# Performance work log

Hardware: AMD Instinct MI355X
Metric: run time of the kernel (lower is better)

## Reference

```python
import jax, jax.numpy as jnp
import numpy as np

E, D_MODEL, D_HIDDEN, N_TOKENS = 8, 1024, 4096, 16384


def setup_inputs() -> dict:
    key = jax.random.key(0)
    ks = jax.random.split(key, 6)
    inp = {
        "hidden_states": jax.random.normal(ks[0], (N_TOKENS, D_MODEL), jnp.float32),
        # tokens are pre-sorted by expert; equal-sized groups of N_TOKENS // E
        "fwd_expert_count": jnp.full((E,), N_TOKENS // E, dtype=jnp.int32),
        # weights stored [E, d_in, d_out] (math-equivalent transpose of torch's [E, out, in])
        "w_gelu": jax.random.normal(ks[1], (E, D_MODEL, D_HIDDEN), jnp.float32) * 0.02,
        "w_lin": jax.random.normal(ks[2], (E, D_MODEL, D_HIDDEN), jnp.float32) * 0.02,
        "b_lin": jax.random.normal(ks[3], (E, D_HIDDEN), jnp.float32) * 0.02,
        "w_o": jax.random.normal(ks[4], (E, D_HIDDEN, D_MODEL), jnp.float32) * 0.02,
        "b_o": jax.random.normal(ks[5], (E, D_MODEL), jnp.float32) * 0.02,
    }
    return inp


def reference(hidden_states, fwd_expert_count, w_gelu, w_lin, b_lin, w_o, b_o):
    # Grouped GEMM MoE expert FFN with gated GELU (T5DenseGatedActDense per expert).
    # setup_inputs uses equal group sizes, so the grouped GEMM is expressed as a
    # batched einsum over [E, capacity, d] blocks (tokens are sorted by expert).
    e, d_model, d_hidden = w_gelu.shape
    n = hidden_states.shape[0]
    cap = n // e  # per-expert token count (== fwd_expert_count[i])
    x = hidden_states.reshape(e, cap, d_model)
    # gate branch: no bias (FMoELinear bias=False), gelu_new (tanh approx)
    hidden_gelu = jax.nn.gelu(jnp.einsum('ecd,edh->ech', x, w_gelu), approximate=True)
    # linear branch: bias=True
    hidden_linear = jnp.einsum('ecd,edh->ech', x, w_lin) + b_lin[:, None, :]
    h = hidden_gelu * hidden_linear  # dropout is identity at inference
    out = jnp.einsum('ech,ehd->ecd', h, w_o) + b_o[:, None, :]
    return out.reshape(n, d_model)
```

## Files before the change

### kernel.cpp

```cpp
#include <hip/hip_runtime.h>

#define EXP 8
#define DM 1024
#define DH 4096
#define NT 16384

typedef __attribute__((ext_vector_type(8))) short bf16x8;
typedef __attribute__((ext_vector_type(4))) float f32x4;

static __device__ __forceinline__ unsigned short f2bf(float f) {
  unsigned int u = __float_as_uint(f);
  u = u + 0x7FFFu + ((u >> 16) & 1u);
  return (unsigned short)(u >> 16);
}

static __device__ __forceinline__ void gload_lds16(const void* g, void* l) {
  __builtin_amdgcn_global_load_lds((const __attribute__((address_space(1))) void*)g,
                                   (__attribute__((address_space(3))) void*)l, 16, 0, 0);
}

__global__ void cvt_bf16_k(const float* __restrict__ in, unsigned short* __restrict__ out,
                           long n4) {
  long i = (long)blockIdx.x * blockDim.x + threadIdx.x;
  const long stride = (long)gridDim.x * blockDim.x;
  for (; i < n4; i += stride) {
    const float4 v = ((const float4*)in)[i];
    ushort4 o;
    o.x = f2bf(v.x); o.y = f2bf(v.y); o.z = f2bf(v.z); o.w = f2bf(v.w);
    ((ushort4*)out)[i] = o;
  }
}

__global__ void transpose_cvt(const float* __restrict__ in, unsigned short* __restrict__ out,
                              int K, int N) {
  __shared__ float tile[32][33];
  const int n0 = blockIdx.x * 32, k0 = blockIdx.y * 32;
  const size_t boff = (size_t)blockIdx.z * K * N;
  const int tx = threadIdx.x, ty = threadIdx.y;
  const float* src = in + boff;
  unsigned short* dst = out + boff;
#pragma unroll
  for (int i = 0; i < 32; i += 8)
    tile[ty + i][tx] = src[(size_t)(k0 + ty + i) * N + n0 + tx];
  __syncthreads();
#pragma unroll
  for (int i = 0; i < 32; i += 8)
    dst[(size_t)(n0 + ty + i) * K + k0 + tx] = f2bf(tile[tx][ty + i]);
}


#define LDSA(row, chunk) lds[sb + (row) * 64 + ((((chunk) ^ ((row) & 7))) << 3)]
#define LDSB(row, chunk) lds[sb + 16384 + (row) * 64 + ((((chunk) ^ ((row) & 7))) << 3)]

#define RD_A(mh)                                                                   \
  _Pragma("unroll") for (int i = 0; i < 4; i++) _Pragma("unroll") for (int ks = 0; \
                                                                       ks < 2;    \
                                                                       ks++)      \
      fa[i][ks] = *(const bf16x8*)&LDSA(wr * 128 + (mh) * 64 + i * 16 + lrow, ks * 4 + khi);

#define RD_B(dst, jb)                                                              \
  _Pragma("unroll") for (int j = 0; j < 2; j++) _Pragma("unroll") for (int ks = 0; \
                                                                       ks < 2;    \
                                                                       ks++)      \
      dst[j][ks] = *(const bf16x8*)&LDSB(wc * 64 + ((jb) + j) * 16 + lrow, ks * 4 + khi);

#define MFMA16(mi, jb, fb)                                                        \
  __builtin_amdgcn_s_setprio(1);                                                  \
  _Pragma("unroll") for (int i = 0; i < 4; i++) _Pragma("unroll") for (int j = 0; \
                                                                       j < 2;    \
                                                                       j++)      \
      _Pragma("unroll") for (int ks = 0; ks < 2; ks++) acc[(mi) + i][(jb) + j] =  \
          __builtin_amdgcn_mfma_f32_16x16x32_bf16(fa[i][ks], fb[j][ks],           \
                                                  acc[(mi) + i][(jb) + j], 0, 0, 0); \
  __builtin_amdgcn_s_setprio(0);

#define BAR_FENCE()                      \
  __builtin_amdgcn_s_barrier();          \
  asm volatile("" ::: "memory");

__global__ __launch_bounds__(512, 1) void gemm1(
    const unsigned short* __restrict__ Xb,
    const unsigned short* __restrict__ WgT,
    const unsigned short* __restrict__ WlT,
    const float* __restrict__ b_lin,
    unsigned short* __restrict__ Hb) {
  __shared__ unsigned short lds[65536];

  const int t = threadIdx.x;
  const int nblk = blockIdx.x, mblk = blockIdx.y;
  const int e = mblk >> 3;
  const int m0 = mblk * 256, n0 = nblk * 128;

  const int lane = t & 63, wave = t >> 6;
  const int wr = wave >> 2, wc = wave & 3;
  const int lrow = lane & 15, khi = lane >> 4;

  const int presw = (((t & 7) ^ ((t >> 3) & 7)) << 3);
  const unsigned short* gAsrc = Xb + (size_t)(m0 + (t >> 3)) * DM + presw;
  const unsigned short* gGsrc = WgT + ((size_t)e * DH + n0 + (t >> 3)) * DM + presw;
  const unsigned short* gLsrc = WlT + ((size_t)e * DH + n0 + (t >> 3)) * DM + presw;

  const int KT = DM / 64;

  auto STAGE_A = [&](int kt, int half) {
    unsigned short* d = &lds[(kt & 1) * 32768 + half * 8192 + t * 8];
    const unsigned short* s = gAsrc + (size_t)(half * 128) * DM + kt * 64;
    gload_lds16(s, d);
    gload_lds16(s + (size_t)64 * DM, d + 4096);
  };
  auto STAGE_B = [&](int kt, int half) {
    unsigned short* d = &lds[(kt & 1) * 32768 + 16384 + half * 8192 + t * 8];
    const unsigned short* s = (half ? gLsrc : gGsrc) + kt * 64;
    gload_lds16(s, d);
    gload_lds16(s + (size_t)64 * DM, d + 4096);
  };

  f32x4 acc[8][4];
#pragma unroll
  for (int m = 0; m < 8; m++)
#pragma unroll
    for (int j = 0; j < 4; j++) acc[m][j] = 0.0f;

  STAGE_A(0, 0); STAGE_A(0, 1);
  STAGE_B(0, 0); STAGE_B(0, 1);
  STAGE_B(1, 0); STAGE_B(1, 1);
  asm volatile("s_waitcnt vmcnt(4)" ::: "memory");
  BAR_FENCE();

  for (int T = 0; T < KT; ++T) {
    const int sb = (T & 1) * 32768;
    bf16x8 fa[4][2], fb01[2][2], fb23[2][2];
    RD_A(0);
    RD_B(fb01, 0);
    if (T + 1 < KT) STAGE_A(T + 1, 0);
    __builtin_amdgcn_s_barrier();
    MFMA16(0, 0, fb01);
    BAR_FENCE();
    RD_B(fb23, 2);
    if (T + 1 < KT) STAGE_A(T + 1, 1);
    __builtin_amdgcn_s_barrier();
    MFMA16(0, 2, fb23);
    BAR_FENCE();
    RD_A(1);
    if (T + 2 < KT) STAGE_B(T + 2, 0);
    __builtin_amdgcn_s_barrier();
    MFMA16(4, 2, fb23);
    BAR_FENCE();
    if (T + 2 < KT) STAGE_B(T + 2, 1);
    __builtin_amdgcn_s_barrier();
    MFMA16(4, 0, fb01);
    if (T < KT - 2)       asm volatile("s_waitcnt vmcnt(4)" ::: "memory");
    else if (T == KT - 2) asm volatile("s_waitcnt vmcnt(0)" ::: "memory");
    BAR_FENCE();
  }

  __syncthreads();
  f32x4* ex = (f32x4*)lds;
  if (wc >= 2) {
    f32x4* dst = ex + (wr * 2 + (wc - 2)) * 2048;
#pragma unroll
    for (int m = 0; m < 8; m++)
#pragma unroll
      for (int j = 0; j < 4; j++) dst[(m * 4 + j) * 64 + lane] = acc[m][j];
  }
  __syncthreads();
  if (wc < 2) {
    const f32x4* src = ex + (wr * 2 + wc) * 2048;
#pragma unroll
    for (int m = 0; m < 8; m++) {
      const int rowbase = m0 + wr * 128 + (m >> 2) * 64 + (m & 3) * 16 + khi * 4;
#pragma unroll
      for (int j = 0; j < 4; j++) {
        const f32x4 l4 = src[(m * 4 + j) * 64 + lane];
        const int gcol = n0 + wc * 64 + j * 16 + lrow;
        const float bias = b_lin[(size_t)e * DH + gcol];
#pragma unroll
        for (int r = 0; r < 4; r++) {
          const float g = acc[m][j][r];
          const float li = l4[r] + bias;
          const float u = 0.7978845608028654f * (g + 0.044715f * g * g * g);
          const float th = 1.0f - 2.0f / (1.0f + __expf(2.0f * u));
          const float h = 0.5f * g * (1.0f + th) * li;
          Hb[(size_t)(rowbase + r) * DH + gcol] = f2bf(h);
        }
      }
    }
  }
}

__global__ __launch_bounds__(512, 1) void gemm2(
    const unsigned short* __restrict__ Hb,
    const unsigned short* __restrict__ WoT,
    const float* __restrict__ b_o,
    float* __restrict__ out) {
  __shared__ unsigned short lds[65536];

  const int t = threadIdx.x;
  const int nblk = blockIdx.x, mblk = blockIdx.y;
  const int e = mblk >> 3;
  const int m0 = mblk * 256, n0 = nblk * 256;

  const int lane = t & 63, wave = t >> 6;
  const int wr = wave >> 2, wc = wave & 3;
  const int lrow = lane & 15, khi = lane >> 4;

  const int presw = (((t & 7) ^ ((t >> 3) & 7)) << 3);
  const unsigned short* gAsrc = Hb + (size_t)(m0 + (t >> 3)) * DH + presw;
  const unsigned short* gBsrc = WoT + ((size_t)e * DM + n0 + (t >> 3)) * DH + presw;

  const int KT = DH / 64;

  auto STAGE_A = [&](int kt, int half) {
    unsigned short* d = &lds[(kt & 1) * 32768 + half * 8192 + t * 8];
    const unsigned short* s = gAsrc + (size_t)(half * 128) * DH + kt * 64;
    gload_lds16(s, d);
    gload_lds16(s + (size_t)64 * DH, d + 4096);
  };
  auto STAGE_B = [&](int kt, int half) {
    unsigned short* d = &lds[(kt & 1) * 32768 + 16384 + half * 8192 + t * 8];
    const unsigned short* s = gBsrc + (size_t)(half * 128) * DH + kt * 64;
    gload_lds16(s, d);
    gload_lds16(s + (size_t)64 * DH, d + 4096);
  };

  f32x4 acc[8][4];
#pragma unroll
  for (int m = 0; m < 8; m++)
#pragma unroll
    for (int j = 0; j < 4; j++) acc[m][j] = 0.0f;

  STAGE_A(0, 0); STAGE_A(0, 1);
  STAGE_B(0, 0); STAGE_B(0, 1);
  STAGE_B(1, 0); STAGE_B(1, 1);
  asm volatile("s_waitcnt vmcnt(4)" ::: "memory");
  BAR_FENCE();

  for (int T = 0; T < KT; ++T) {
    const int sb = (T & 1) * 32768;
    bf16x8 fa[4][2], fb01[2][2], fb23[2][2];
    RD_A(0);
    RD_B(fb01, 0);
    if (T + 1 < KT) STAGE_A(T + 1, 0);
    __builtin_amdgcn_s_barrier();
    MFMA16(0, 0, fb01);
    BAR_FENCE();
    RD_B(fb23, 2);
    if (T + 1 < KT) STAGE_A(T + 1, 1);
    __builtin_amdgcn_s_barrier();
    MFMA16(0, 2, fb23);
    BAR_FENCE();
    RD_A(1);
    if (T + 2 < KT) STAGE_B(T + 2, 0);
    __builtin_amdgcn_s_barrier();
    MFMA16(4, 2, fb23);
    BAR_FENCE();
    if (T + 2 < KT) STAGE_B(T + 2, 1);
    __builtin_amdgcn_s_barrier();
    MFMA16(4, 0, fb01);
    if (T < KT - 2)       asm volatile("s_waitcnt vmcnt(4)" ::: "memory");
    else if (T == KT - 2) asm volatile("s_waitcnt vmcnt(0)" ::: "memory");
    BAR_FENCE();
  }

  const float* bop = b_o + (size_t)e * DM;
#pragma unroll
  for (int m = 0; m < 8; m++) {
    const int rowbase = m0 + wr * 128 + (m >> 2) * 64 + (m & 3) * 16 + khi * 4;
#pragma unroll
    for (int j = 0; j < 4; j++) {
      const int gcol = n0 + wc * 64 + j * 16 + lrow;
      const float bias = bop[gcol];
#pragma unroll
      for (int r = 0; r < 4; r++)
        out[(size_t)(rowbase + r) * DM + gcol] = acc[m][j][r] + bias;
    }
  }
}

extern "C" void kernel_launch(void* const* d_in, const int* in_sizes, int n_in,
                              void* d_out, int out_size, void* d_ws, size_t ws_size,
                              hipStream_t stream) {
  const float* hs = (const float*)d_in[0];
  const float* w_gelu = (const float*)d_in[2];
  const float* w_lin = (const float*)d_in[3];
  const float* b_lin = (const float*)d_in[4];
  const float* w_o = (const float*)d_in[5];
  const float* b_o = (const float*)d_in[6];
  float* outp = (float*)d_out;

  unsigned short* Xb = (unsigned short*)d_ws;
  unsigned short* WgT = Xb + (size_t)NT * DM;
  unsigned short* WlT = WgT + (size_t)EXP * DH * DM;
  unsigned short* WoT = WlT + (size_t)EXP * DH * DM;
  unsigned short* Hb = WoT + (size_t)EXP * DH * DM;

  cvt_bf16_k<<<dim3(2048), dim3(256), 0, stream>>>(hs, Xb, (long)NT * DM / 4);
  transpose_cvt<<<dim3(DH / 32, DM / 32, EXP), dim3(32, 8), 0, stream>>>(w_gelu, WgT, DM, DH);
  transpose_cvt<<<dim3(DH / 32, DM / 32, EXP), dim3(32, 8), 0, stream>>>(w_lin, WlT, DM, DH);
  transpose_cvt<<<dim3(DM / 32, DH / 32, EXP), dim3(32, 8), 0, stream>>>(w_o, WoT, DH, DM);

  gemm1<<<dim3(DH / 128, NT / 256), dim3(512), 0, stream>>>(Xb, WgT, WlT, b_lin, Hb);
  gemm2<<<dim3(DM / 256, NT / 256), dim3(512), 0, stream>>>(Hb, WoT, b_o, outp);
}
```

Baseline: 612.2 us.

## Replace pipelined gemm1 with simpler single-buffered 128x128 tile kernel

Rewrites the gate/linear GEMM kernel to use 256-thread blocks with 128x128 tiles, separate gate and linear accumulators per wave, and a plain load-sync-compute loop. It drops the double-buffered, barrier-interleaved software pipeline and the LDS exchange in the epilogue. The aim is higher occupancy (two blocks per CU) and a simpler epilogue. In exchange it loses the overlap of global loads with MFMA work and increases global traffic through smaller tiles.

```diff
diff --git a/kernel.cpp b/kernel.cpp
--- a/kernel.cpp
+++ b/kernel.cpp
@@ -17,6 +17,10 @@
 static __device__ __forceinline__ void gload_lds16(const void* g, void* l) {
   __builtin_amdgcn_global_load_lds((const __attribute__((address_space(1))) void*)g,
                                    (__attribute__((address_space(3))) void*)l, 16, 0, 0);
+}
+
+static __device__ __forceinline__ int swz_idx(int r, int kk) {
+  return r * 64 + (((kk >> 3) ^ (r & 7)) << 3);
 }
 
 __global__ void cvt_bf16_k(const float* __restrict__ in, unsigned short* __restrict__ out,
@@ -48,6 +52,96 @@
     dst[(size_t)(n0 + ty + i) * K + k0 + tx] = f2bf(tile[tx][ty + i]);
 }
 
+__global__ __launch_bounds__(256, 2) void gemm1(
+    const unsigned short* __restrict__ Xb,
+    const unsigned short* __restrict__ WgT,
+    const unsigned short* __restrict__ WlT,
+    const float* __restrict__ b_lin,
+    unsigned short* __restrict__ Hb) {
+  __shared__ unsigned short sA[128 * 64];
+  __shared__ unsigned short sBg[128 * 64];
+  __shared__ unsigned short sBl[128 * 64];
+
+  const int t = threadIdx.x;
+  const int nblk = blockIdx.x, mblk = blockIdx.y;
+  const int e = mblk >> 4;
+  const int m0 = mblk * 128, n0 = nblk * 128;
+
+  const int lane = t & 63;
+  const int wave = t >> 6;
+  const int wr = wave >> 1, wc = wave & 1;
+  const int lrow = lane & 15;
+  const int lk8 = (lane >> 4) * 8;
+
+  const int srow = t >> 3;
+  const int schunk = t & 7;
+  const int ssw = ((schunk ^ (srow & 7)) << 3);
+
+  const unsigned short* gA = Xb + (size_t)m0 * DM + ssw;
+  const unsigned short* gG = WgT + (size_t)e * DH * DM + (size_t)n0 * DM + ssw;
+  const unsigned short* gL = WlT + (size_t)e * DH * DM + (size_t)n0 * DM + ssw;
+
+  f32x4 accg[4][4], accl[4][4];
+#pragma unroll
+  for (int i = 0; i < 4; i++)
+#pragma unroll
+    for (int j = 0; j < 4; j++) { accg[i][j] = 0.0f; accl[i][j] = 0.0f; }
+
+  for (int kt = 0; kt < DM / 64; ++kt) {
+    const int k0 = kt * 64;
+#pragma unroll
+    for (int c = 0; c < 4; c++) {
+      const int row = c * 32 + srow;
+      gload_lds16(gA + (size_t)row * DM + k0, (char*)sA + row * 128 + schunk * 16);
+      gload_lds16(gG + (size_t)row * DM + k0, (char*)sBg + row * 128 + schunk * 16);
+      gload_lds16(gL + (size_t)row * DM + k0, (char*)sBl + row * 128 + schunk * 16);
+    }
+    __syncthreads();
+#pragma unroll
+    for (int ks = 0; ks < 2; ks++) {
+      const int kk = ks * 32 + lk8;
+      bf16x8 af[4], bg[4], bl[4];
+#pragma unroll
+      for (int i = 0; i < 4; i++)
+        af[i] = *(const bf16x8*)&sA[swz_idx(wr * 64 + i * 16 + lrow, kk)];
+#pragma unroll
+      for (int j = 0; j < 4; j++) {
+        bg[j] = *(const bf16x8*)&sBg[swz_idx(wc * 64 + j * 16 + lrow, kk)];
+        bl[j] = *(const bf16x8*)&sBl[swz_idx(wc * 64 + j * 16 + lrow, kk)];
+      }
+#pragma unroll
+      for (int i = 0; i < 4; i++)
+#pragma unroll
+        for (int j = 0; j < 4; j++) {
+          accg[i][j] = __builtin_amdgcn_mfma_f32_16x16x32_bf16(af[i], bg[j], accg[i][j], 0, 0, 0);
+          accl[i][j] = __builtin_amdgcn_mfma_f32_16x16x32_bf16(af[i], bl[j], accl[i][j], 0, 0, 0);
+        }
+    }
+    __syncthreads();
+  }
+
+  const float* bl_p = b_lin + (size_t)e * DH;
+  const int r0 = (lane >> 4) * 4;
+#pragma unroll
+  for (int i = 0; i < 4; i++) {
+    const int grow = m0 + wr * 64 + i * 16 + r0;
+#pragma unroll
+    for (int j = 0; j < 4; j++) {
+      const int gcol = n0 + wc * 64 + j * 16 + lrow;
+      const float bias = bl_p[gcol];
+#pragma unroll
+      for (int r = 0; r < 4; r++) {
+        const float g = accg[i][j][r];
+        const float li = accl[i][j][r] + bias;
+        const float u = 0.7978845608028654f * (g + 0.044715f * g * g * g);
+        const float th = 1.0f - 2.0f / (1.0f + __expf(2.0f * u));
+        const float h = 0.5f * g * (1.0f + th) * li;
+        Hb[(size_t)(grow + r) * DH + gcol] = f2bf(h);
+      }
+    }
+  }
+}
+
 
 #define LDSA(row, chunk) lds[sb + (row) * 64 + ((((chunk) ^ ((row) & 7))) << 3)]
 #define LDSB(row, chunk) lds[sb + 16384 + (row) * 64 + ((((chunk) ^ ((row) & 7))) << 3)]
@@ -77,116 +171,6 @@
 #define BAR_FENCE()                      \
   __builtin_amdgcn_s_barrier();          \
   asm volatile("" ::: "memory");
-
-__global__ __launch_bounds__(512, 1) void gemm1(
-    const unsigned short* __restrict__ Xb,
-    const unsigned short* __restrict__ WgT,
-    const unsigned short* __restrict__ WlT,
-    const float* __restrict__ b_lin,
-    unsigned short* __restrict__ Hb) {
-  __shared__ unsigned short lds[65536];
-
-  const int t = threadIdx.x;
-  const int nblk = blockIdx.x, mblk = blockIdx.y;
-  const int e = mblk >> 3;
-  const int m0 = mblk * 256, n0 = nblk * 128;
-
-  const int lane = t & 63, wave = t >> 6;
-  const int wr = wave >> 2, wc = wave & 3;
-  const int lrow = lane & 15, khi = lane >> 4;
-
-  const int presw = (((t & 7) ^ ((t >> 3) & 7)) << 3);
-  const unsigned short* gAsrc = Xb + (size_t)(m0 + (t >> 3)) * DM + presw;
-  const unsigned short* gGsrc = WgT + ((size_t)e * DH + n0 + (t >> 3)) * DM + presw;
-  const unsigned short* gLsrc = WlT + ((size_t)e * DH + n0 + (t >> 3)) * DM + presw;
-
-  const int KT = DM / 64;
-
-  auto STAGE_A = [&](int kt, int half) {
-    unsigned short* d = &lds[(kt & 1) * 32768 + half * 8192 + t * 8];
-    const unsigned short* s = gAsrc + (size_t)(half * 128) * DM + kt * 64;
-    gload_lds16(s, d);
-    gload_lds16(s + (size_t)64 * DM, d + 4096);
-  };
-  auto STAGE_B = [&](int kt, int half) {
-    unsigned short* d = &lds[(kt & 1) * 32768 + 16384 + half * 8192 + t * 8];
-    const unsigned short* s = (half ? gLsrc : gGsrc) + kt * 64;
-    gload_lds16(s, d);
-    gload_lds16(s + (size_t)64 * DM, d + 4096);
-  };
-
-  f32x4 acc[8][4];
-#pragma unroll
-  for (int m = 0; m < 8; m++)
-#pragma unroll
-    for (int j = 0; j < 4; j++) acc[m][j] = 0.0f;
-
-  STAGE_A(0, 0); STAGE_A(0, 1);
-  STAGE_B(0, 0); STAGE_B(0, 1);
-  STAGE_B(1, 0); STAGE_B(1, 1);
-  asm volatile("s_waitcnt vmcnt(4)" ::: "memory");
-  BAR_FENCE();
-
-  for (int T = 0; T < KT; ++T) {
-    const int sb = (T & 1) * 32768;
-    bf16x8 fa[4][2], fb01[2][2], fb23[2][2];
-    RD_A(0);
-    RD_B(fb01, 0);
-    if (T + 1 < KT) STAGE_A(T + 1, 0);
-    __builtin_amdgcn_s_barrier();
-    MFMA16(0, 0, fb01);
-    BAR_FENCE();
-    RD_B(fb23, 2);
-    if (T + 1 < KT) STAGE_A(T + 1, 1);
-    __builtin_amdgcn_s_barrier();
-    MFMA16(0, 2, fb23);
-    BAR_FENCE();
-    RD_A(1);
-    if (T + 2 < KT) STAGE_B(T + 2, 0);
-    __builtin_amdgcn_s_barrier();
-    MFMA16(4, 2, fb23);
-    BAR_FENCE();
-    if (T + 2 < KT) STAGE_B(T + 2, 1);
-    __builtin_amdgcn_s_barrier();
-    MFMA16(4, 0, fb01);
-    if (T < KT - 2)       asm volatile("s_waitcnt vmcnt(4)" ::: "memory");
-    else if (T == KT - 2) asm volatile("s_waitcnt vmcnt(0)" ::: "memory");
-    BAR_FENCE();
-  }
-
-  __syncthreads();
-  f32x4* ex = (f32x4*)lds;
-  if (wc >= 2) {
-    f32x4* dst = ex + (wr * 2 + (wc - 2)) * 2048;
-#pragma unroll
-    for (int m = 0; m < 8; m++)
-#pragma unroll
-      for (int j = 0; j < 4; j++) dst[(m * 4 + j) * 64 + lane] = acc[m][j];
-  }
-  __syncthreads();
-  if (wc < 2) {
-    const f32x4* src = ex + (wr * 2 + wc) * 2048;
-#pragma unroll
-    for (int m = 0; m < 8; m++) {
-      const int rowbase = m0 + wr * 128 + (m >> 2) * 64 + (m & 3) * 16 + khi * 4;
-#pragma unroll
-      for (int j = 0; j < 4; j++) {
-        const f32x4 l4 = src[(m * 4 + j) * 64 + lane];
-        const int gcol = n0 + wc * 64 + j * 16 + lrow;
-        const float bias = b_lin[(size_t)e * DH + gcol];
-#pragma unroll
-        for (int r = 0; r < 4; r++) {
-          const float g = acc[m][j][r];
-          const float li = l4[r] + bias;
-          const float u = 0.7978845608028654f * (g + 0.044715f * g * g * g);
-          const float th = 1.0f - 2.0f / (1.0f + __expf(2.0f * u));
-          const float h = 0.5f * g * (1.0f + th) * li;
-          Hb[(size_t)(rowbase + r) * DH + gcol] = f2bf(h);
-        }
-      }
-    }
-  }
-}
 
 __global__ __launch_bounds__(512, 1) void gemm2(
     const unsigned short* __restrict__ Hb,
@@ -299,6 +283,6 @@
   transpose_cvt<<<dim3(DH / 32, DM / 32, EXP), dim3(32, 8), 0, stream>>>(w_lin, WlT, DM, DH);
   transpose_cvt<<<dim3(DM / 32, DH / 32, EXP), dim3(32, 8), 0, stream>>>(w_o, WoT, DH, DM);
 
-  gemm1<<<dim3(DH / 128, NT / 256), dim3(512), 0, stream>>>(Xb, WgT, WlT, b_lin, Hb);
+  gemm1<<<dim3(DH / 128, NT / 128), dim3(256), 0, stream>>>(Xb, WgT, WlT, b_lin, Hb);
   gemm2<<<dim3(DM / 256, NT / 256), dim3(512), 0, stream>>>(Hb, WoT, b_o, outp);
 }
```

Result: faster. 588.7 us (-3.8%).

## Interleave gate/linear weights per 16 columns and vectorize weight transpose

Applied to the files above, without the earlier changes.

Weight prep now writes gate and linear weights into one interleaved buffer in alternating 16-column groups. gemm1 can then load a single 256-wide B tile and combine gate and linear results inside each wave's registers, with no LDS exchange. This removes the post-loop LDS round trip and the half-idle epilogue where only half the waves wrote output. The transpose kernels move to 64x64 tiles with float4 loads and ushort4 stores, which should cut prep cost but adds LDS bank-conflict risk on the strided tile reads.

```diff
diff --git a/kernel.cpp b/kernel.cpp
--- a/kernel.cpp
+++ b/kernel.cpp
@@ -31,21 +31,66 @@
   }
 }
 
-__global__ void transpose_cvt(const float* __restrict__ in, unsigned short* __restrict__ out,
-                              int K, int N) {
-  __shared__ float tile[32][33];
-  const int n0 = blockIdx.x * 32, k0 = blockIdx.y * 32;
-  const size_t boff = (size_t)blockIdx.z * K * N;
-  const int tx = threadIdx.x, ty = threadIdx.y;
-  const float* src = in + boff;
-  unsigned short* dst = out + boff;
-#pragma unroll
-  for (int i = 0; i < 32; i += 8)
-    tile[ty + i][tx] = src[(size_t)(k0 + ty + i) * N + n0 + tx];
+__global__ void transpose_cvt64(const float* __restrict__ src0,
+                                unsigned short* __restrict__ dst0, int K, int N) {
+  __shared__ float tile[64][65];
+  const int t = threadIdx.x;
+  const int tx = t & 15, ty = t >> 4;
+  const int n0 = blockIdx.x * 64, k0 = blockIdx.y * 64;
+  const int z = blockIdx.z;
+  const float* src = src0 + (size_t)z * K * N;
+  unsigned short* dst = dst0 + (size_t)z * K * N;
+#pragma unroll
+  for (int i = 0; i < 64; i += 16) {
+    const float4 v = *(const float4*)&src[(size_t)(k0 + ty + i) * N + n0 + tx * 4];
+    tile[ty + i][tx * 4 + 0] = v.x;
+    tile[ty + i][tx * 4 + 1] = v.y;
+    tile[ty + i][tx * 4 + 2] = v.z;
+    tile[ty + i][tx * 4 + 3] = v.w;
+  }
   __syncthreads();
 #pragma unroll
-  for (int i = 0; i < 32; i += 8)
-    dst[(size_t)(n0 + ty + i) * K + k0 + tx] = f2bf(tile[tx][ty + i]);
+  for (int i = 0; i < 64; i += 16) {
+    ushort4 o;
+    o.x = f2bf(tile[tx * 4 + 0][ty + i]);
+    o.y = f2bf(tile[tx * 4 + 1][ty + i]);
+    o.z = f2bf(tile[tx * 4 + 2][ty + i]);
+    o.w = f2bf(tile[tx * 4 + 3][ty + i]);
+    *(ushort4*)&dst[(size_t)(n0 + ty + i) * K + k0 + tx * 4] = o;
+  }
+}
+
+__global__ void transpose_cvt64_il(const float* __restrict__ w_gelu,
+                                   const float* __restrict__ w_lin,
+                                   unsigned short* __restrict__ W1T) {
+  __shared__ float tile[64][65];
+  const int t = threadIdx.x;
+  const int tx = t & 15, ty = t >> 4;
+  const int n0 = blockIdx.x * 64, k0 = blockIdx.y * 64;
+  const int z = blockIdx.z;
+  const int gl16 = (z >> 3) * 16;
+  const float* src = (z >> 3 ? w_lin : w_gelu) + (size_t)(z & 7) * DM * DH;
+  unsigned short* dst = W1T + (size_t)(z & 7) * 2 * DH * DM;
+#pragma unroll
+  for (int i = 0; i < 64; i += 16) {
+    const float4 v = *(const float4*)&src[(size_t)(k0 + ty + i) * DH + n0 + tx * 4];
+    tile[ty + i][tx * 4 + 0] = v.x;
+    tile[ty + i][tx * 4 + 1] = v.y;
+    tile[ty + i][tx * 4 + 2] = v.z;
+    tile[ty + i][tx * 4 + 3] = v.w;
+  }
+  __syncthreads();
+#pragma unroll
+  for (int i = 0; i < 64; i += 16) {
+    const int n = n0 + ty + i;
+    const int rowI = ((n >> 4) << 5) + (n & 15) + gl16;
+    ushort4 o;
+    o.x = f2bf(tile[tx * 4 + 0][ty + i]);
+    o.y = f2bf(tile[tx * 4 + 1][ty + i]);
+    o.z = f2bf(tile[tx * 4 + 2][ty + i]);
+    o.w = f2bf(tile[tx * 4 + 3][ty + i]);
+    *(ushort4*)&dst[(size_t)rowI * DM + k0 + tx * 4] = o;
+  }
 }
 
 
@@ -78,10 +123,42 @@
   __builtin_amdgcn_s_barrier();          \
   asm volatile("" ::: "memory");
 
+#define PIPE_LOOP(KT)                                                   \
+  STAGE_A(0, 0); STAGE_A(0, 1);                                         \
+  STAGE_B(0, 0); STAGE_B(0, 1);                                         \
+  STAGE_B(1, 0); STAGE_B(1, 1);                                         \
+  asm volatile("s_waitcnt vmcnt(4)" ::: "memory");                      \
+  BAR_FENCE();                                                          \
+  for (int T = 0; T < (KT); ++T) {                                      \
+    const int sb = (T & 1) * 32768;                                     \
+    bf16x8 fa[4][2], fb01[2][2], fb23[2][2];                            \
+    RD_A(0);                                                            \
+    RD_B(fb01, 0);                                                      \
+    if (T + 1 < (KT)) STAGE_A(T + 1, 0);                                \
+    __builtin_amdgcn_s_barrier();                                       \
+    MFMA16(0, 0, fb01);                                                 \
+    BAR_FENCE();                                                        \
+    RD_B(fb23, 2);                                                      \
+    if (T + 1 < (KT)) STAGE_A(T + 1, 1);                                \
+    __builtin_amdgcn_s_barrier();                                       \
+    MFMA16(0, 2, fb23);                                                 \
+    BAR_FENCE();                                                        \
+    RD_A(1);                                                            \
+    if (T + 2 < (KT)) STAGE_B(T + 2, 0);                                \
+    __builtin_amdgcn_s_barrier();                                       \
+    MFMA16(4, 2, fb23);                                                 \
+    BAR_FENCE();                                                        \
+    if (T + 2 < (KT)) STAGE_B(T + 2, 1);                                \
+    __builtin_amdgcn_s_barrier();                                       \
+    MFMA16(4, 0, fb01);                                                 \
+    if (T < (KT)-2)        asm volatile("s_waitcnt vmcnt(4)" ::: "memory"); \
+    else if (T == (KT)-2)  asm volatile("s_waitcnt vmcnt(0)" ::: "memory"); \
+    BAR_FENCE();                                                        \
+  }
+
 __global__ __launch_bounds__(512, 1) void gemm1(
     const unsigned short* __restrict__ Xb,
-    const unsigned short* __restrict__ WgT,
-    const unsigned short* __restrict__ WlT,
+    const unsigned short* __restrict__ W1T,
     const float* __restrict__ b_lin,
     unsigned short* __restrict__ Hb) {
   __shared__ unsigned short lds[65536];
@@ -89,7 +166,7 @@
   const int t = threadIdx.x;
   const int nblk = blockIdx.x, mblk = blockIdx.y;
   const int e = mblk >> 3;
-  const int m0 = mblk * 256, n0 = nblk * 128;
+  const int m0 = mblk * 256, n0 = nblk * 256;
 
   const int lane = t & 63, wave = t >> 6;
   const int wr = wave >> 2, wc = wave & 3;
@@ -97,10 +174,7 @@
 
   const int presw = (((t & 7) ^ ((t >> 3) & 7)) << 3);
   const unsigned short* gAsrc = Xb + (size_t)(m0 + (t >> 3)) * DM + presw;
-  const unsigned short* gGsrc = WgT + ((size_t)e * DH + n0 + (t >> 3)) * DM + presw;
-  const unsigned short* gLsrc = WlT + ((size_t)e * DH + n0 + (t >> 3)) * DM + presw;
-
-  const int KT = DM / 64;
+  const unsigned short* gBsrc = W1T + ((size_t)e * 2 * DH + n0 + (t >> 3)) * DM + presw;
 
   auto STAGE_A = [&](int kt, int half) {
     unsigned short* d = &lds[(kt & 1) * 32768 + half * 8192 + t * 8];
@@ -110,7 +184,7 @@
   };
   auto STAGE_B = [&](int kt, int half) {
     unsigned short* d = &lds[(kt & 1) * 32768 + 16384 + half * 8192 + t * 8];
-    const unsigned short* s = (half ? gLsrc : gGsrc) + kt * 64;
+    const unsigned short* s = gBsrc + (size_t)(half * 128) * DM + kt * 64;
     gload_lds16(s, d);
     gload_lds16(s + (size_t)64 * DM, d + 4096);
   };
@@ -121,68 +195,23 @@
 #pragma unroll
     for (int j = 0; j < 4; j++) acc[m][j] = 0.0f;
 
-  STAGE_A(0, 0); STAGE_A(0, 1);
-  STAGE_B(0, 0); STAGE_B(0, 1);
-  STAGE_B(1, 0); STAGE_B(1, 1);
-  asm volatile("s_waitcnt vmcnt(4)" ::: "memory");
-  BAR_FENCE();
-
-  for (int T = 0; T < KT; ++T) {
-    const int sb = (T & 1) * 32768;
-    bf16x8 fa[4][2], fb01[2][2], fb23[2][2];
-    RD_A(0);
-    RD_B(fb01, 0);
-    if (T + 1 < KT) STAGE_A(T + 1, 0);
-    __builtin_amdgcn_s_barrier();
-    MFMA16(0, 0, fb01);
-    BAR_FENCE();
-    RD_B(fb23, 2);
-    if (T + 1 < KT) STAGE_A(T + 1, 1);
-    __builtin_amdgcn_s_barrier();
-    MFMA16(0, 2, fb23);
-    BAR_FENCE();
-    RD_A(1);
-    if (T + 2 < KT) STAGE_B(T + 2, 0);
-    __builtin_amdgcn_s_barrier();
-    MFMA16(4, 2, fb23);
-    BAR_FENCE();
-    if (T + 2 < KT) STAGE_B(T + 2, 1);
-    __builtin_amdgcn_s_barrier();
-    MFMA16(4, 0, fb01);
-    if (T < KT - 2)       asm volatile("s_waitcnt vmcnt(4)" ::: "memory");
-    else if (T == KT - 2) asm volatile("s_waitcnt vmcnt(0)" ::: "memory");
-    BAR_FENCE();
-  }
-
-  __syncthreads();
-  f32x4* ex = (f32x4*)lds;
-  if (wc >= 2) {
-    f32x4* dst = ex + (wr * 2 + (wc - 2)) * 2048;
-#pragma unroll
-    for (int m = 0; m < 8; m++)
-#pragma unroll
-      for (int j = 0; j < 4; j++) dst[(m * 4 + j) * 64 + lane] = acc[m][j];
-  }
-  __syncthreads();
-  if (wc < 2) {
-    const f32x4* src = ex + (wr * 2 + wc) * 2048;
-#pragma unroll
-    for (int m = 0; m < 8; m++) {
-      const int rowbase = m0 + wr * 128 + (m >> 2) * 64 + (m & 3) * 16 + khi * 4;
-#pragma unroll
-      for (int j = 0; j < 4; j++) {
-        const f32x4 l4 = src[(m * 4 + j) * 64 + lane];
-        const int gcol = n0 + wc * 64 + j * 16 + lrow;
-        const float bias = b_lin[(size_t)e * DH + gcol];
-#pragma unroll
-        for (int r = 0; r < 4; r++) {
-          const float g = acc[m][j][r];
-          const float li = l4[r] + bias;
-          const float u = 0.7978845608028654f * (g + 0.044715f * g * g * g);
-          const float th = 1.0f - 2.0f / (1.0f + __expf(2.0f * u));
-          const float h = 0.5f * g * (1.0f + th) * li;
-          Hb[(size_t)(rowbase + r) * DH + gcol] = f2bf(h);
-        }
+  PIPE_LOOP(DM / 64);
+
+#pragma unroll
+  for (int m = 0; m < 8; m++) {
+    const int rowbase = m0 + wr * 128 + (m >> 2) * 64 + (m & 3) * 16 + khi * 4;
+#pragma unroll
+    for (int p = 0; p < 2; p++) {
+      const int hcol = nblk * 128 + (2 * wc + p) * 16 + lrow;
+      const float bias = b_lin[(size_t)e * DH + hcol];
+#pragma unroll
+      for (int r = 0; r < 4; r++) {
+        const float g = acc[m][2 * p][r];
+        const float li = acc[m][2 * p + 1][r] + bias;
+        const float u = 0.7978845608028654f * (g + 0.044715f * g * g * g);
+        const float th = 1.0f - 2.0f / (1.0f + __expf(2.0f * u));
+        const float h = 0.5f * g * (1.0f + th) * li;
+        Hb[(size_t)(rowbase + r) * DH + hcol] = f2bf(h);
       }
     }
   }
@@ -208,8 +237,6 @@
   const unsigned short* gAsrc = Hb + (size_t)(m0 + (t >> 3)) * DH + presw;
   const unsigned short* gBsrc = WoT + ((size_t)e * DM + n0 + (t >> 3)) * DH + presw;
 
-  const int KT = DH / 64;
-
   auto STAGE_A = [&](int kt, int half) {
     unsigned short* d = &lds[(kt & 1) * 32768 + half * 8192 + t * 8];
     const unsigned short* s = gAsrc + (size_t)(half * 128) * DH + kt * 64;
@@ -229,38 +256,7 @@
 #pragma unroll
     for (int j = 0; j < 4; j++) acc[m][j] = 0.0f;
 
-  STAGE_A(0, 0); STAGE_A(0, 1);
-  STAGE_B(0, 0); STAGE_B(0, 1);
-  STAGE_B(1, 0); STAGE_B(1, 1);
-  asm volatile("s_waitcnt vmcnt(4)" ::: "memory");
-  BAR_FENCE();
-
-  for (int T = 0; T < KT; ++T) {
-    const int sb = (T & 1) * 32768;
-    bf16x8 fa[4][2], fb01[2][2], fb23[2][2];
-    RD_A(0);
-    RD_B(fb01, 0);
-    if (T + 1 < KT) STAGE_A(T + 1, 0);
-    __builtin_amdgcn_s_barrier();
-    MFMA16(0, 0, fb01);
-    BAR_FENCE();
-    RD_B(fb23, 2);
-    if (T + 1 < KT) STAGE_A(T + 1, 1);
-    __builtin_amdgcn_s_barrier();
-    MFMA16(0, 2, fb23);
-    BAR_FENCE();
-    RD_A(1);
-    if (T + 2 < KT) STAGE_B(T + 2, 0);
-    __builtin_amdgcn_s_barrier();
-    MFMA16(4, 2, fb23);
-    BAR_FENCE();
-    if (T + 2 < KT) STAGE_B(T + 2, 1);
-    __builtin_amdgcn_s_barrier();
-    MFMA16(4, 0, fb01);
-    if (T < KT - 2)       asm volatile("s_waitcnt vmcnt(4)" ::: "memory");
-    else if (T == KT - 2) asm volatile("s_waitcnt vmcnt(0)" ::: "memory");
-    BAR_FENCE();
-  }
+  PIPE_LOOP(DH / 64);
 
   const float* bop = b_o + (size_t)e * DM;
 #pragma unroll
@@ -289,16 +285,15 @@
   float* outp = (float*)d_out;
 
   unsigned short* Xb = (unsigned short*)d_ws;
-  unsigned short* WgT = Xb + (size_t)NT * DM;
-  unsigned short* WlT = WgT + (size_t)EXP * DH * DM;
-  unsigned short* WoT = WlT + (size_t)EXP * DH * DM;
+  unsigned short* W1T = Xb + (size_t)NT * DM;
+  unsigned short* WoT = W1T + (size_t)EXP * 2 * DH * DM;
   unsigned short* Hb = WoT + (size_t)EXP * DH * DM;
 
   cvt_bf16_k<<<dim3(2048), dim3(256), 0, stream>>>(hs, Xb, (long)NT * DM / 4);
-  transpose_cvt<<<dim3(DH / 32, DM / 32, EXP), dim3(32, 8), 0, stream>>>(w_gelu, WgT, DM, DH);
-  transpose_cvt<<<dim3(DH / 32, DM / 32, EXP), dim3(32, 8), 0, stream>>>(w_lin, WlT, DM, DH);
-  transpose_cvt<<<dim3(DM / 32, DH / 32, EXP), dim3(32, 8), 0, stream>>>(w_o, WoT, DH, DM);
-
-  gemm1<<<dim3(DH / 128, NT / 256), dim3(512), 0, stream>>>(Xb, WgT, WlT, b_lin, Hb);
+  transpose_cvt64_il<<<dim3(DH / 64, DM / 64, 16), dim3(256), 0, stream>>>(
+      w_gelu, w_lin, W1T);
+  transpose_cvt64<<<dim3(DM / 64, DH / 64, 8), dim3(256), 0, stream>>>(w_o, WoT, DH, DM);
+
+  gemm1<<<dim3(2 * DH / 256, NT / 256), dim3(512), 0, stream>>>(Xb, W1T, b_lin, Hb);
   gemm2<<<dim3(DM / 256, NT / 256), dim3(512), 0, stream>>>(Hb, WoT, b_o, outp);
 }
```

Result: faster. 559.3 us, median of 2 (-8.6%).
